# Kernel optimization log

Measured on AMD Instinct MI355X. Metric: run time of the kernel, lower is better.

## Reference

```python
import jax, jax.numpy as jnp
import numpy as np

N = 32768          # nodes
E = 131072         # edges
H = 4              # heads
RNA = 128          # rna_feature_dim
PROT = 32          # prot_feature_dim
F0 = 64            # num_features_per_layer[0] == [1]
CIN = F0 + PROT    # cross-path feature dim (96)
LRELU = 0.2


def _param(key, shape):
    return jax.random.normal(key, shape, dtype=jnp.float32) * 0.1


def setup_inputs() -> dict:
    key = jax.random.key(0)
    ks = jax.random.split(key, 20)
    return {
        "rna_data": jax.random.normal(ks[0], (N, RNA), dtype=jnp.float32),
        "prot_data": jax.random.normal(ks[1], (N, PROT), dtype=jnp.float32),
        "edge_index": jax.random.randint(ks[2], (2, E), 0, N, dtype=jnp.int32),
        "W_gat_proj": _param(ks[3], (RNA, F0)),
        "b_gat_proj": _param(ks[4], (F0,)),
        "W_gat_reproj": _param(ks[5], (F0, RNA)),
        "b_gat_reproj": _param(ks[6], (RNA,)),
        "Wg": _param(ks[7], (F0, H * F0)),
        "ag_src": _param(ks[8], (H, F0)),
        "ag_trg": _param(ks[9], (H, F0)),
        "bg": _param(ks[10], (F0,)),
        "W_cross_proj": _param(ks[11], (RNA + PROT, CIN)),
        "b_cross_proj": _param(ks[12], (CIN,)),
        "W_cross_reproj": _param(ks[13], (CIN, RNA + PROT)),
        "b_cross_reproj": _param(ks[14], (RNA + PROT,)),
        "Wc": _param(ks[15], (CIN, H * CIN)),
        "ac_src": _param(ks[16], (H, CIN)),
        "ac_trg": _param(ks[17], (H, CIN)),
        "bc": _param(ks[18], (CIN,)),
    }


def gat_layer(x, W, a_src, a_trg, bias, edge_index, softmax_on_src):
    """GATLayer with concat=False, activation=None, skip connection (in==out dim),
    dropout in eval mode. CrossAttnLayer groups the edge-softmax by src instead of trg."""
    n, f = x.shape
    src, trg = edge_index[0], edge_index[1]
    proj = (x @ W).reshape(n, H, f)                               # [N,H,F] lift targets
    s_src = jnp.einsum('nhf,hf->nh', proj, a_src)                 # [N,H]
    s_trg = jnp.einsum('nhf,hf->nh', proj, a_trg)                 # [N,H]
    scores = jax.nn.leaky_relu(s_src[src] + s_trg[trg], LRELU)    # [E,H] per-edge scores
    grp = src if softmax_on_src else trg
    ex = jnp.exp(scores - scores.max())                           # global-max shift (as in source)
    denom = jax.ops.segment_sum(ex, grp, num_segments=n)          # [N,H]
    attn = ex / (denom[grp] + 1e-16)                              # neighborhood-aware softmax [E,H]
    weighted = proj[src] * attn[:, :, None]                       # [E,H,F]
    out = jax.ops.segment_sum(weighted, trg, num_segments=n)      # scatter-add aggregate [N,H,F]
    out = out + x[:, None, :]                                     # direct skip (out_dim == in_dim)
    out = out.mean(axis=1) + bias                                 # concat=False -> head mean, + bias
    return out                                                    # activation=None (last layer)


def reference(rna_data, prot_data, edge_index,
              W_gat_proj, b_gat_proj, W_gat_reproj, b_gat_reproj,
              Wg, ag_src, ag_trg, bg,
              W_cross_proj, b_cross_proj, W_cross_reproj, b_cross_reproj,
              Wc, ac_src, ac_trg, bc):
    concat = jnp.concatenate([rna_data, prot_data], axis=1)       # [N, RNA+PROT]
    rna_p = rna_data @ W_gat_proj + b_gat_proj                    # [N, F0]
    cross_p = concat @ W_cross_proj + b_cross_proj                # [N, CIN]
    gat_out = gat_layer(rna_p, Wg, ag_src, ag_trg, bg, edge_index, False)    # [N, F0]
    cross_out = gat_layer(cross_p, Wc, ac_src, ac_trg, bc, edge_index, True)  # [N, CIN]
    # CrossAttnLayer's trailing view(-1, num_heads, num_out_features)
    cross_out = cross_out.reshape(-1, H, CIN)                     # [N/H, H, CIN]
    gat_final = gat_out @ W_gat_reproj + b_gat_reproj             # [N, RNA]
    cross_final = cross_out @ W_cross_reproj + b_cross_reproj     # [N/H, H, RNA+PROT]
    return gat_final, cross_final
```

## Files before the change

### kernel.cpp

```cpp
#include <hip/hip_runtime.h>
#include <hip/hip_bf16.h>

#define NN 32768
#define NE 131072
#define HH 4

constexpr float kLrelu = 0.2f;

using bf16x8 = __attribute__((ext_vector_type(8))) __bf16;
using f32x4  = __attribute__((ext_vector_type(4))) float;

__device__ inline short f2b(float f) {
    __hip_bfloat16 h = __float2bfloat16(f);
    return __builtin_bit_cast(short, h);
}
__device__ inline float b2f(short s) {
    __hip_bfloat16 h = __builtin_bit_cast(__hip_bfloat16, s);
    return __bfloat162float(h);
}
__device__ inline float blo(int u) {
    return __builtin_bit_cast(float, (int)(u << 16));
}
__device__ inline float bhi(int u) {
    return __builtin_bit_cast(float, (int)(u & 0xffff0000));
}
__device__ inline float lrexp(float x) {
    return __expf(x > 0.f ? x : kLrelu * x);
}

template<int K, int LDA, int OUTN, int BM, int BN, bool BF16OUT>
__device__ __forceinline__ void gemm_dev(
    const short* __restrict__ A, const short* __restrict__ Wt,
    const float* __restrict__ bias,
    float* __restrict__ Cf, short* __restrict__ Cb,
    short* lds, int bx, int by)
{
    constexpr int KP    = K + 8;
    constexpr int WM    = BM / 32;
    constexpr int WN    = 4 / WM;
    constexpr int WBN   = BN / WN;
    constexpr int CF    = WBN / 16;
    constexpr int CPR   = K / 8;
    constexpr int TOT   = (BM + BN) * KP;
    constexpr int SLICE = TOT / 4;

    short* As = lds;
    short* Bs = lds + BM * KP;

    const int tid  = threadIdx.x;
    const int wave = tid >> 6;
    const int lane = tid & 63;
    const int lr   = lane & 15;
    const int kb   = lane >> 4;
    const int wm   = wave % WM;
    const int wn   = wave / WM;
    const int row0 = bx * BM;
    const int col0 = by * BN;

    #pragma unroll
    for (int g = tid; g < BM * CPR; g += 256) {
        int r = g / CPR, c = g - r * CPR;
        bf16x8 v = *(const bf16x8*)(A + (size_t)(row0 + r) * LDA + c * 8);
        *(bf16x8*)(As + r * KP + c * 8) = v;
    }
    #pragma unroll
    for (int g = tid; g < BN * CPR; g += 256) {
        int r = g / CPR, c = g - r * CPR;
        bf16x8 v = *(const bf16x8*)(Wt + (size_t)(col0 + r) * K + c * 8);
        *(bf16x8*)(Bs + r * KP + c * 8) = v;
    }
    __syncthreads();

    f32x4 acc[2][CF] = {};
    #pragma unroll
    for (int k0 = 0; k0 < K; k0 += 32) {
        bf16x8 af0 = *(const bf16x8*)(As + (wm * 32 + lr     ) * KP + k0 + kb * 8);
        bf16x8 af1 = *(const bf16x8*)(As + (wm * 32 + lr + 16) * KP + k0 + kb * 8);
        #pragma unroll
        for (int cf = 0; cf < CF; ++cf) {
            bf16x8 bv = *(const bf16x8*)(Bs + (wn * WBN + cf * 16 + lr) * KP + k0 + kb * 8);
            acc[0][cf] = __builtin_amdgcn_mfma_f32_16x16x32_bf16(af0, bv, acc[0][cf], 0, 0, 0);
            acc[1][cf] = __builtin_amdgcn_mfma_f32_16x16x32_bf16(af1, bv, acc[1][cf], 0, 0, 0);
        }
    }

    #pragma unroll
    for (int mf = 0; mf < 2; ++mf) {
        __syncthreads();
        if constexpr (BF16OUT) {
            constexpr int LEP = WBN + 8;
            short* ep = lds + wave * SLICE;
            #pragma unroll
            for (int cf = 0; cf < CF; ++cf) {
                const int c  = cf * 16 + lr;
                const float bv = bias ? bias[col0 + wn * WBN + c] : 0.0f;
                #pragma unroll
                for (int j = 0; j < 4; ++j)
                    ep[(kb * 4 + j) * LEP + c] = f2b(acc[mf][cf][j] + bv);
            }
            __syncthreads();
            constexpr int CROW = WBN / 8;
            for (int g = lane; g < 16 * CROW; g += 64) {
                int r = g / CROW, cc = g - r * CROW;
                bf16x8 v = *(const bf16x8*)(ep + r * LEP + cc * 8);
                *(bf16x8*)(Cb + (size_t)(row0 + wm * 32 + mf * 16 + r) * OUTN
                              + col0 + wn * WBN + cc * 8) = v;
            }
        } else {
            constexpr int LEPF = WBN + 4;
            float* epf = (float*)(lds + wave * SLICE);
            #pragma unroll
            for (int cf = 0; cf < CF; ++cf) {
                const int c  = cf * 16 + lr;
                const float bv = bias ? bias[col0 + wn * WBN + c] : 0.0f;
                #pragma unroll
                for (int j = 0; j < 4; ++j)
                    epf[(kb * 4 + j) * LEPF + c] = acc[mf][cf][j] + bv;
            }
            __syncthreads();
            constexpr int CROWF = WBN / 4;
            for (int g = lane; g < 16 * CROWF; g += 64) {
                int r = g / CROWF, cc = g - r * CROWF;
                float4 v = *(const float4*)(epf + r * LEPF + cc * 4);
                *(float4*)(Cf + (size_t)(row0 + wm * 32 + mf * 16 + r) * OUTN
                              + col0 + wn * WBN + cc * 4) = v;
            }
        }
    }
}

template<int K1, int LDA1, int OUTN1, int BM1, int BN1, bool BO1,
         int K2, int LDA2, int OUTN2, int BM2, int BN2, bool BO2>
__global__ __launch_bounds__(256) void dual_gemm(
    const short* A1, const short* Wt1, const float* b1, float* Cf1, short* Cb1,
    int nbx1, int nby1,
    const short* A2, const short* Wt2, const float* b2, float* Cf2, short* Cb2,
    int nbx2, int nby2)
{
    constexpr int TOT1 = (BM1 + BN1) * (K1 + 8);
    constexpr int TOT2 = (BM2 + BN2) * (K2 + 8);
    constexpr int TOT  = TOT1 > TOT2 ? TOT1 : TOT2;
    __shared__ short lds[TOT];
    if (blockIdx.z == 0) {
        if ((int)blockIdx.x < nbx1 && (int)blockIdx.y < nby1)
            gemm_dev<K1, LDA1, OUTN1, BM1, BN1, BO1>(A1, Wt1, b1, Cf1, Cb1, lds,
                                                     blockIdx.x, blockIdx.y);
    } else {
        if ((int)blockIdx.x < nbx2 && (int)blockIdx.y < nby2)
            gemm_dev<K2, LDA2, OUTN2, BM2, BN2, BO2>(A2, Wt2, b2, Cf2, Cb2, lds,
                                                     blockIdx.x, blockIdx.y);
    }
}

template<int F>
__device__ inline void score_one(
    const short* __restrict__ proj_b,
    const float* __restrict__ a_src, const float* __restrict__ a_trg,
    float* __restrict__ ssrc, float* __restrict__ strg, int t)
{
    int n = t >> 2, h = t & 3;
    const int4* p = (const int4*)(proj_b + (size_t)n * (4 * F) + h * F);
    const float* as = a_src + h * F;
    const float* at = a_trg + h * F;
    float ss = 0.f, st = 0.f;
    #pragma unroll
    for (int c = 0; c < F / 8; ++c) {
        int4 v = p[c];
        int u[4] = { v.x, v.y, v.z, v.w };
        #pragma unroll
        for (int q = 0; q < 4; ++q) {
            float x0 = blo(u[q]), x1 = bhi(u[q]);
            ss += x0 * as[c * 8 + 2 * q] + x1 * as[c * 8 + 2 * q + 1];
            st += x0 * at[c * 8 + 2 * q] + x1 * at[c * 8 + 2 * q + 1];
        }
    }
    ssrc[t] = ss;
    strg[t] = st;
}

__global__ __launch_bounds__(256) void scores_both(
    const short* __restrict__ projG,
    const float* __restrict__ agsG, const float* __restrict__ agtG,
    float* __restrict__ ssrcG, float* __restrict__ strgG,
    const short* __restrict__ projC,
    const float* __restrict__ acsC, const float* __restrict__ actC,
    float* __restrict__ ssrcC, float* __restrict__ strgC)
{
    int t = blockIdx.x * 256 + threadIdx.x;
    if (t < NN * HH) score_one<64>(projG, agsG, agtG, ssrcG, strgG, t);
    else             score_one<96>(projC, acsC, actC, ssrcC, strgC, t - NN * HH);
}

__global__ __launch_bounds__(256) void prep_kernel(
    const float* __restrict__ rna, const float* __restrict__ prot,
    short* __restrict__ cb,
    const float* W0, const float* W1, const float* W2,
    const float* W3, const float* W4, const float* W5,
    short* T0, short* T1, short* T2, short* T3, short* T4, short* T5,
    int4* __restrict__ zero_p)
{
    const int bid = blockIdx.x;
    if (bid < 5120) {
        int t = bid * 256 + threadIdx.x;
        int n = t / 40, j = (t - n * 40) * 4;
        float4 v = (j < 128) ? *(const float4*)(rna  + (size_t)n * 128 + j)
                             : *(const float4*)(prot + (size_t)n * 32 + (j - 128));
        short4 o = { f2b(v.x), f2b(v.y), f2b(v.z), f2b(v.w) };
        *(short4*)(cb + (size_t)n * 160 + j) = o;
    } else if (bid < 5984) {
        int idx = bid - 5120;
        int wsel = idx / 144, sub = idx - wsel * 144;
        int K, N; const float* W; short* T;
        switch (wsel) {
            case 0: K = 128; N =  64; W = W0; T = T0; break;
            case 1: K =  64; N = 256; W = W1; T = T1; break;
            case 2: K =  64; N = 128; W = W2; T = T2; break;
            case 3: K = 160; N =  96; W = W3; T = T3; break;
            case 4: K =  96; N = 384; W = W4; T = T4; break;
            default:K =  96; N = 160; W = W5; T = T5; break;
        }
        int t = sub * 256 + threadIdx.x;
        if (t >= K * N) return;
        int n = t / K, k = t - n * K;
        T[t] = f2b(W[(size_t)k * N + n]);
    } else {
        zero_p[(bid - 5984) * 256 + threadIdx.x] = make_int4(0, 0, 0, 0);
    }
}

__global__ __launch_bounds__(256) void hist_dual(const int* __restrict__ ei,
                                                 int* __restrict__ deg_t,
                                                 int* __restrict__ deg_s)
{
    int e = blockIdx.x * 256 + threadIdx.x;
    if (e >= NE) return;
    atomicAdd(&deg_s[ei[e]], 1);
    atomicAdd(&deg_t[ei[NE + e]], 1);
}

__global__ __launch_bounds__(1024) void scan_dual(
    const int* __restrict__ deg_t, int* __restrict__ rowptr_t, int* __restrict__ cursor_t,
    const int* __restrict__ deg_s, int* __restrict__ rowptr_s, int* __restrict__ cursor_s)
{
    const int* deg    = blockIdx.x ? deg_s    : deg_t;
    int*       rowptr = blockIdx.x ? rowptr_s : rowptr_t;
    int*       cursor = blockIdx.x ? cursor_s : cursor_t;
    __shared__ int sums[1024];
    const int t = threadIdx.x;
    const int base = t * 32;
    int local[32];
    int s = 0;
    #pragma unroll
    for (int i = 0; i < 32; ++i) { local[i] = s; s += deg[base + i]; }
    sums[t] = s;
    __syncthreads();
    for (int off = 1; off < 1024; off <<= 1) {
        int v = (t >= off) ? sums[t - off] : 0;
        __syncthreads();
        sums[t] += v;
        __syncthreads();
    }
    const int prev = (t == 0) ? 0 : sums[t - 1];
    #pragma unroll
    for (int i = 0; i < 32; ++i) {
        rowptr[base + i] = prev + local[i];
        cursor[base + i] = prev + local[i];
    }
    if (t == 1023) rowptr[NN] = prev + s;
}

__global__ __launch_bounds__(256) void scatter_dual(
    const int* __restrict__ ei,
    int* __restrict__ cursor_t, int* __restrict__ csr_srcT,
    int* __restrict__ cursor_s, int* __restrict__ csr_trgS)
{
    int e = blockIdx.x * 256 + threadIdx.x;
    if (e >= NE) return;
    int s = ei[e], t = ei[NE + e];
    int st = atomicAdd(&cursor_t[t], 1);
    csr_srcT[st] = s;
    int ss = atomicAdd(&cursor_s[s], 1);
    csr_trgS[ss] = t;
}

__global__ __launch_bounds__(256) void den_src_kernel(
    const int* __restrict__ rowptr_s, const int* __restrict__ csr_trgS,
    const float* __restrict__ ssrc, const float* __restrict__ strg,
    float* __restrict__ recip)
{
    int n = blockIdx.x * 256 + threadIdx.x;
    if (n >= NN) return;
    const int beg = rowptr_s[n], end = rowptr_s[n + 1];
    const float4 sv = *(const float4*)(ssrc + 4 * (size_t)n);
    float d0 = 0.f, d1 = 0.f, d2 = 0.f, d3 = 0.f;
    for (int sl = beg; sl < end; ++sl) {
        const int t = csr_trgS[sl];
        const float4 tv = *(const float4*)(strg + 4 * (size_t)t);
        d0 += lrexp(sv.x + tv.x); d1 += lrexp(sv.y + tv.y);
        d2 += lrexp(sv.z + tv.z); d3 += lrexp(sv.w + tv.w);
    }
    *(float4*)(recip + 4 * (size_t)n) =
        make_float4(1.f / (d0 + 1e-16f), 1.f / (d1 + 1e-16f),
                    1.f / (d2 + 1e-16f), 1.f / (d3 + 1e-16f));
}

template<int F, bool GROUP_SRC>
__device__ __forceinline__ void agg_body(
    int f2, int node,
    const int* __restrict__ rowptr_t, const int* __restrict__ csr_srcT,
    const float* __restrict__ ssrc, const float* __restrict__ strg,
    const float* __restrict__ recip,
    const short* __restrict__ proj_b,
    const short* __restrict__ x_pb, const float* __restrict__ bias,
    short* __restrict__ aggb)
{
    const int beg = rowptr_t[node], end = rowptr_t[node + 1];
    const float4 stv = *(const float4*)(strg + 4 * (size_t)node);

    float a0 = 0.f, a1 = 0.f;
    float h0l = 0.f, h1l = 0.f, h2l = 0.f, h3l = 0.f;
    float h0h = 0.f, h1h = 0.f, h2h = 0.f, h3h = 0.f;
    float d0 = 0.f, d1 = 0.f, d2 = 0.f, d3 = 0.f;

    #pragma unroll 2
    for (int sl = beg; sl < end; ++sl) {
        const int s = csr_srcT[sl];
        const float4 sv = *(const float4*)(ssrc + 4 * (size_t)s);
        float e0 = lrexp(sv.x + stv.x);
        float e1 = lrexp(sv.y + stv.y);
        float e2 = lrexp(sv.z + stv.z);
        float e3 = lrexp(sv.w + stv.w);
        const short* p = proj_b + (size_t)s * (4 * F) + f2;
        const int u0 = *(const int*)(p);
        const int u1 = *(const int*)(p + F);
        const int u2 = *(const int*)(p + 2 * F);
        const int u3 = *(const int*)(p + 3 * F);
        if constexpr (GROUP_SRC) {
            const float4 rc = *(const float4*)(recip + 4 * (size_t)s);
            e0 *= rc.x; e1 *= rc.y; e2 *= rc.z; e3 *= rc.w;
            a0 += e0 * blo(u0) + e1 * blo(u1) + e2 * blo(u2) + e3 * blo(u3);
            a1 += e0 * bhi(u0) + e1 * bhi(u1) + e2 * bhi(u2) + e3 * bhi(u3);
        } else {
            d0 += e0; d1 += e1; d2 += e2; d3 += e3;
            h0l += e0 * blo(u0); h0h += e0 * bhi(u0);
            h1l += e1 * blo(u1); h1h += e1 * bhi(u1);
            h2l += e2 * blo(u2); h2h += e2 * bhi(u2);
            h3l += e3 * blo(u3); h3h += e3 * bhi(u3);
        }
    }
    if constexpr (!GROUP_SRC) {
        const float r0 = 1.f / (d0 + 1e-16f), r1 = 1.f / (d1 + 1e-16f);
        const float r2 = 1.f / (d2 + 1e-16f), r3 = 1.f / (d3 + 1e-16f);
        a0 = h0l * r0 + h1l * r1 + h2l * r2 + h3l * r3;
        a1 = h0h * r0 + h1h * r1 + h2h * r2 + h3h * r3;
    }
    const int o = node * F + f2;
    const int ux = *(const int*)(x_pb + o);
    const float v0 = a0 * 0.25f + blo(ux) + bias[f2];
    const float v1 = a1 * 0.25f + bhi(ux) + bias[f2 + 1];
    *(int*)(aggb + o) = (f2b(v0) & 0xffff) | ((int)f2b(v1) << 16);
}

#define GAT_BLKS 2731
__global__ __launch_bounds__(384) void aggregate_mega(
    const int* __restrict__ rowptr_t, const int* __restrict__ csr_srcT,
    const float* __restrict__ ssrcG, const float* __restrict__ strgG,
    const float* __restrict__ ssrcC, const float* __restrict__ strgC,
    const float* __restrict__ recip,
    const short* __restrict__ projG, const short* __restrict__ projC,
    const short* __restrict__ xG, const short* __restrict__ xC,
    const float* __restrict__ biasG, const float* __restrict__ biasC,
    short* __restrict__ aggG, short* __restrict__ aggC)
{
    const int bid = blockIdx.x;
    const int tid = threadIdx.x;
    if (bid < GAT_BLKS) {
        const int node = bid * 12 + tid / 32;
        const int f2   = (tid & 31) * 2;
        if (node >= NN) return;
        agg_body<64, false>(f2, node, rowptr_t, csr_srcT, ssrcG, strgG,
                            nullptr, projG, xG, biasG, aggG);
    } else {
        const int b    = bid - GAT_BLKS;
        const int node = b * 8 + tid / 48;
        const int f2   = (tid % 48) * 2;
        agg_body<96, true>(f2, node, rowptr_t, csr_srcT, ssrcC, strgC,
                           recip, projC, xC, biasC, aggC);
    }
}

extern "C" void kernel_launch(void* const* d_in, const int* in_sizes, int n_in,
                              void* d_out, int out_size, void* d_ws, size_t ws_size,
                              hipStream_t stream)
{
    const float* rna   = (const float*)d_in[0];
    const float* prot  = (const float*)d_in[1];
    const int*   ei    = (const int*)  d_in[2];
    const float* Wgp   = (const float*)d_in[3];
    const float* bgp   = (const float*)d_in[4];
    const float* Wgr   = (const float*)d_in[5];
    const float* bgr   = (const float*)d_in[6];
    const float* Wg    = (const float*)d_in[7];
    const float* ags   = (const float*)d_in[8];
    const float* agt   = (const float*)d_in[9];
    const float* bg    = (const float*)d_in[10];
    const float* Wcp   = (const float*)d_in[11];
    const float* bcp   = (const float*)d_in[12];
    const float* Wcr   = (const float*)d_in[13];
    const float* bcr   = (const float*)d_in[14];
    const float* Wc    = (const float*)d_in[15];
    const float* acs   = (const float*)d_in[16];
    const float* act   = (const float*)d_in[17];
    const float* bc    = (const float*)d_in[18];

    float* out_gat   = (float*)d_out;
    float* out_cross = out_gat + (size_t)NN * 128;

    float* ssrcG  = (float*)d_ws;
    float* strgG  = ssrcG + (size_t)NN * 4;
    float* ssrcC  = strgG + (size_t)NN * 4;
    float* strgC  = ssrcC + (size_t)NN * 4;
    float* recip  = strgC + (size_t)NN * 4;
    short* projG  = (short*)(recip + (size_t)NN * 4);
    short* projC  = projG + (size_t)NN * 256;
    short* cb     = projC + (size_t)NN * 384;
    short* x_pG   = cb    + (size_t)NN * 160;
    short* x_pC   = x_pG  + (size_t)NN * 64;
    short* aggG   = x_pC  + (size_t)NN * 96;
    short* aggC   = aggG  + (size_t)NN * 64;
    short* wt_gp  = aggC  + (size_t)NN * 96;
    short* wt_g   = wt_gp + 128 * 64;
    short* wt_gr  = wt_g  + 64 * 256;
    short* wt_cp  = wt_gr + 64 * 128;
    short* wt_c   = wt_cp + 160 * 96;
    short* wt_cr  = wt_c  + 96 * 384;
    int*   deg_t  = (int*)(wt_cr + 96 * 160);
    int*   deg_s  = deg_t  + NN;
    int*   cursor_t = deg_s  + NN;
    int*   cursor_s = cursor_t + NN;
    int*   rowptr_t = cursor_s + NN;
    int*   rowptr_s = rowptr_t + NN + 1;
    int*   csr_srcT = rowptr_s + NN + 1;
    int*   csr_trgS = csr_srcT + NE;

    prep_kernel<<<6048, 256, 0, stream>>>(rna, prot, cb,
                                          Wgp, Wg, Wgr, Wcp, Wc, Wcr,
                                          wt_gp, wt_g, wt_gr, wt_cp, wt_c, wt_cr,
                                          (int4*)deg_t);
    hist_dual<<<NE / 256, 256, 0, stream>>>(ei, deg_t, deg_s);
    scan_dual<<<2, 1024, 0, stream>>>(deg_t, rowptr_t, cursor_t, deg_s, rowptr_s, cursor_s);
    scatter_dual<<<NE / 256, 256, 0, stream>>>(ei, cursor_t, csr_srcT, cursor_s, csr_trgS);

    dual_gemm<128, 160,  64, 32,  64, true,
              160, 160,  96, 64,  96, true><<<dim3(1024, 1, 2), 256, 0, stream>>>(
        cb, wt_gp, bgp, nullptr, x_pG, 1024, 1,
        cb, wt_cp, bcp, nullptr, x_pC,  512, 1);

    dual_gemm< 64,  64, 256, 64, 128, true,
               96,  96, 384, 64, 128, true><<<dim3(512, 3, 2), 256, 0, stream>>>(
        x_pG, wt_g, nullptr, nullptr, projG, 512, 2,
        x_pC, wt_c, nullptr, nullptr, projC, 512, 3);

    scores_both<<<(2 * NN * HH) / 256, 256, 0, stream>>>(
        projG, ags, agt, ssrcG, strgG, projC, acs, act, ssrcC, strgC);
    den_src_kernel<<<NN / 256, 256, 0, stream>>>(rowptr_s, csr_trgS, ssrcC, strgC, recip);

    aggregate_mega<<<GAT_BLKS + NN / 8, 384, 0, stream>>>(
        rowptr_t, csr_srcT, ssrcG, strgG, ssrcC, strgC, recip,
        projG, projC, x_pG, x_pC, bg, bc, aggG, aggC);

    dual_gemm< 64,  64, 128, 64,  64, false,
               96,  96, 160, 64, 160, false><<<dim3(512, 2, 2), 256, 0, stream>>>(
        aggG, wt_gr, bgr, out_gat,   nullptr, 512, 2,
        aggC, wt_cr, bcr, out_cross, nullptr, 512, 1);
}
```

Before: 167.2 us.

## Split each node's edge loop across two thread halves in aggregation

The aggregation kernel now assigns two groups of lanes per node, each handling alternate incoming edges, then combines partial sums (via cross-lane shuffle for the GAT path and shared memory plus a block barrier for the cross path). This doubles the thread count and block count to expose more memory-level parallelism on the irregular gather. In exchange it adds reduction overhead, a __syncthreads, and half the lanes idle during the epilogue.

```diff
diff --git a/kernel.cpp b/kernel.cpp
--- a/kernel.cpp
+++ b/kernel.cpp
@@ -304,64 +304,7 @@
                     1.f / (d2 + 1e-16f), 1.f / (d3 + 1e-16f));
 }
 
-template<int F, bool GROUP_SRC>
-__device__ __forceinline__ void agg_body(
-    int f2, int node,
-    const int* __restrict__ rowptr_t, const int* __restrict__ csr_srcT,
-    const float* __restrict__ ssrc, const float* __restrict__ strg,
-    const float* __restrict__ recip,
-    const short* __restrict__ proj_b,
-    const short* __restrict__ x_pb, const float* __restrict__ bias,
-    short* __restrict__ aggb)
-{
-    const int beg = rowptr_t[node], end = rowptr_t[node + 1];
-    const float4 stv = *(const float4*)(strg + 4 * (size_t)node);
-
-    float a0 = 0.f, a1 = 0.f;
-    float h0l = 0.f, h1l = 0.f, h2l = 0.f, h3l = 0.f;
-    float h0h = 0.f, h1h = 0.f, h2h = 0.f, h3h = 0.f;
-    float d0 = 0.f, d1 = 0.f, d2 = 0.f, d3 = 0.f;
-
-    #pragma unroll 2
-    for (int sl = beg; sl < end; ++sl) {
-        const int s = csr_srcT[sl];
-        const float4 sv = *(const float4*)(ssrc + 4 * (size_t)s);
-        float e0 = lrexp(sv.x + stv.x);
-        float e1 = lrexp(sv.y + stv.y);
-        float e2 = lrexp(sv.z + stv.z);
-        float e3 = lrexp(sv.w + stv.w);
-        const short* p = proj_b + (size_t)s * (4 * F) + f2;
-        const int u0 = *(const int*)(p);
-        const int u1 = *(const int*)(p + F);
-        const int u2 = *(const int*)(p + 2 * F);
-        const int u3 = *(const int*)(p + 3 * F);
-        if constexpr (GROUP_SRC) {
-            const float4 rc = *(const float4*)(recip + 4 * (size_t)s);
-            e0 *= rc.x; e1 *= rc.y; e2 *= rc.z; e3 *= rc.w;
-            a0 += e0 * blo(u0) + e1 * blo(u1) + e2 * blo(u2) + e3 * blo(u3);
-            a1 += e0 * bhi(u0) + e1 * bhi(u1) + e2 * bhi(u2) + e3 * bhi(u3);
-        } else {
-            d0 += e0; d1 += e1; d2 += e2; d3 += e3;
-            h0l += e0 * blo(u0); h0h += e0 * bhi(u0);
-            h1l += e1 * blo(u1); h1h += e1 * bhi(u1);
-            h2l += e2 * blo(u2); h2h += e2 * bhi(u2);
-            h3l += e3 * blo(u3); h3h += e3 * bhi(u3);
-        }
-    }
-    if constexpr (!GROUP_SRC) {
-        const float r0 = 1.f / (d0 + 1e-16f), r1 = 1.f / (d1 + 1e-16f);
-        const float r2 = 1.f / (d2 + 1e-16f), r3 = 1.f / (d3 + 1e-16f);
-        a0 = h0l * r0 + h1l * r1 + h2l * r2 + h3l * r3;
-        a1 = h0h * r0 + h1h * r1 + h2h * r2 + h3h * r3;
-    }
-    const int o = node * F + f2;
-    const int ux = *(const int*)(x_pb + o);
-    const float v0 = a0 * 0.25f + blo(ux) + bias[f2];
-    const float v1 = a1 * 0.25f + bhi(ux) + bias[f2 + 1];
-    *(int*)(aggb + o) = (f2b(v0) & 0xffff) | ((int)f2b(v1) << 16);
-}
-
-#define GAT_BLKS 2731
+#define GAT_BLKS 5462
 __global__ __launch_bounds__(384) void aggregate_mega(
     const int* __restrict__ rowptr_t, const int* __restrict__ csr_srcT,
     const float* __restrict__ ssrcG, const float* __restrict__ strgG,
@@ -372,20 +315,97 @@
     const float* __restrict__ biasG, const float* __restrict__ biasC,
     short* __restrict__ aggG, short* __restrict__ aggC)
 {
+    __shared__ float red[2][192];
     const int bid = blockIdx.x;
     const int tid = threadIdx.x;
+
     if (bid < GAT_BLKS) {
-        const int node = bid * 12 + tid / 32;
-        const int f2   = (tid & 31) * 2;
+        const int node = bid * 6 + (tid >> 6);
         if (node >= NN) return;
-        agg_body<64, false>(f2, node, rowptr_t, csr_srcT, ssrcG, strgG,
-                            nullptr, projG, xG, biasG, aggG);
+        const int lane = tid & 63;
+        const int half = lane >> 5;
+        const int f2   = (lane & 31) * 2;
+        const int beg  = rowptr_t[node], end = rowptr_t[node + 1];
+        const float4 stv = *(const float4*)(strgG + 4 * (size_t)node);
+
+        float h0l = 0.f, h1l = 0.f, h2l = 0.f, h3l = 0.f;
+        float h0h = 0.f, h1h = 0.f, h2h = 0.f, h3h = 0.f;
+        float d0 = 0.f, d1 = 0.f, d2 = 0.f, d3 = 0.f;
+
+        for (int sl = beg + half; sl < end; sl += 2) {
+            const int s = csr_srcT[sl];
+            const float4 sv = *(const float4*)(ssrcG + 4 * (size_t)s);
+            const float e0 = lrexp(sv.x + stv.x);
+            const float e1 = lrexp(sv.y + stv.y);
+            const float e2 = lrexp(sv.z + stv.z);
+            const float e3 = lrexp(sv.w + stv.w);
+            const short* p = projG + (size_t)s * 256 + f2;
+            const int u0 = *(const int*)(p);
+            const int u1 = *(const int*)(p + 64);
+            const int u2 = *(const int*)(p + 128);
+            const int u3 = *(const int*)(p + 192);
+            d0 += e0; d1 += e1; d2 += e2; d3 += e3;
+            h0l += e0 * blo(u0); h0h += e0 * bhi(u0);
+            h1l += e1 * blo(u1); h1h += e1 * bhi(u1);
+            h2l += e2 * blo(u2); h2h += e2 * bhi(u2);
+            h3l += e3 * blo(u3); h3h += e3 * bhi(u3);
+        }
+        d0 += __shfl_xor(d0, 32); d1 += __shfl_xor(d1, 32);
+        d2 += __shfl_xor(d2, 32); d3 += __shfl_xor(d3, 32);
+        h0l += __shfl_xor(h0l, 32); h0h += __shfl_xor(h0h, 32);
+        h1l += __shfl_xor(h1l, 32); h1h += __shfl_xor(h1h, 32);
+        h2l += __shfl_xor(h2l, 32); h2h += __shfl_xor(h2h, 32);
+        h3l += __shfl_xor(h3l, 32); h3h += __shfl_xor(h3h, 32);
+        if (half == 0) {
+            const float r0 = 1.f / (d0 + 1e-16f), r1 = 1.f / (d1 + 1e-16f);
+            const float r2 = 1.f / (d2 + 1e-16f), r3 = 1.f / (d3 + 1e-16f);
+            const float a0 = h0l * r0 + h1l * r1 + h2l * r2 + h3l * r3;
+            const float a1 = h0h * r0 + h1h * r1 + h2h * r2 + h3h * r3;
+            const int o = node * 64 + f2;
+            const int ux = *(const int*)(xG + o);
+            const float v0 = a0 * 0.25f + blo(ux) + biasG[f2];
+            const float v1 = a1 * 0.25f + bhi(ux) + biasG[f2 + 1];
+            *(int*)(aggG + o) = (f2b(v0) & 0xffff) | ((int)f2b(v1) << 16);
+        }
     } else {
         const int b    = bid - GAT_BLKS;
-        const int node = b * 8 + tid / 48;
-        const int f2   = (tid % 48) * 2;
-        agg_body<96, true>(f2, node, rowptr_t, csr_srcT, ssrcC, strgC,
-                           recip, projC, xC, biasC, aggC);
+        const int nl   = tid / 96;
+        const int r    = tid - nl * 96;
+        const int half = r / 48;
+        const int f2   = (r - half * 48) * 2;
+        const int node = b * 4 + nl;
+        const int beg  = rowptr_t[node], end = rowptr_t[node + 1];
+        const float4 stv = *(const float4*)(strgC + 4 * (size_t)node);
+
+        float a0 = 0.f, a1 = 0.f;
+        for (int sl = beg + half; sl < end; sl += 2) {
+            const int s = csr_srcT[sl];
+            const float4 sv = *(const float4*)(ssrcC + 4 * (size_t)s);
+            const float4 rc = *(const float4*)(recip + 4 * (size_t)s);
+            const float e0 = lrexp(sv.x + stv.x) * rc.x;
+            const float e1 = lrexp(sv.y + stv.y) * rc.y;
+            const float e2 = lrexp(sv.z + stv.z) * rc.z;
+            const float e3 = lrexp(sv.w + stv.w) * rc.w;
+            const short* p = projC + (size_t)s * 384 + f2;
+            const int u0 = *(const int*)(p);
+            const int u1 = *(const int*)(p + 96);
+            const int u2 = *(const int*)(p + 192);
+            const int u3 = *(const int*)(p + 288);
+            a0 += e0 * blo(u0) + e1 * blo(u1) + e2 * blo(u2) + e3 * blo(u3);
+            a1 += e0 * bhi(u0) + e1 * bhi(u1) + e2 * bhi(u2) + e3 * bhi(u3);
+        }
+        const int slot = nl * 48 + (f2 >> 1);
+        if (half == 1) { red[0][slot] = a0; red[1][slot] = a1; }
+        __syncthreads();
+        if (half == 0) {
+            a0 += red[0][slot];
+            a1 += red[1][slot];
+            const int o = node * 96 + f2;
+            const int ux = *(const int*)(xC + o);
+            const float v0 = a0 * 0.25f + blo(ux) + biasC[f2];
+            const float v1 = a1 * 0.25f + bhi(ux) + biasC[f2 + 1];
+            *(int*)(aggC + o) = (f2b(v0) & 0xffff) | ((int)f2b(v1) << 16);
+        }
     }
 }
 
@@ -465,7 +485,7 @@
         projG, ags, agt, ssrcG, strgG, projC, acs, act, ssrcC, strgC);
     den_src_kernel<<<NN / 256, 256, 0, stream>>>(rowptr_s, csr_trgS, ssrcC, strgC, recip);
 
-    aggregate_mega<<<GAT_BLKS + NN / 8, 384, 0, stream>>>(
+    aggregate_mega<<<GAT_BLKS + NN / 4, 384, 0, stream>>>(
         rowptr_t, csr_srcT, ssrcG, strgG, ssrcC, strgC, recip,
         projG, projC, x_pG, x_pC, bg, bc, aggG, aggC);
 
```

After: 179.0 us. 7.0% more time.

## Precompute normalized per-edge attention coefficients in separate kernel before aggregation

Applied to the files above, without the earlier changes.

Adds an attn_both kernel that computes normalized softmax attention weights per edge, stored in CSR order for both the GAT and cross paths. The aggregation kernel then reads one float4 per edge instead of recomputing exp/leaky-relu and the softmax normalization in every feature lane. The aim is to remove redundant transcendental work that was repeated 32–48 times per edge. In exchange it adds a kernel launch, a second pass over edges for the GAT denominator, and 4 MB of extra global writes and reads.

```diff
diff --git a/kernel.cpp b/kernel.cpp
--- a/kernel.cpp
+++ b/kernel.cpp
@@ -304,55 +304,71 @@
                     1.f / (d2 + 1e-16f), 1.f / (d3 + 1e-16f));
 }
 
-template<int F, bool GROUP_SRC>
-__device__ __forceinline__ void agg_body(
+__global__ __launch_bounds__(256) void attn_both(
+    const int* __restrict__ rowptr_t, const int* __restrict__ csr_srcT,
+    const float* __restrict__ ssrcG, const float* __restrict__ strgG,
+    const float* __restrict__ ssrcC, const float* __restrict__ strgC,
+    const float* __restrict__ recip,
+    float* __restrict__ attnG, float* __restrict__ attnC)
+{
+    const int idx = blockIdx.x * 256 + threadIdx.x;
+    if (idx < NN) {
+        const int n = idx;
+        const int beg = rowptr_t[n], end = rowptr_t[n + 1];
+        const float4 tv = *(const float4*)(strgG + 4 * (size_t)n);
+        float d0 = 0.f, d1 = 0.f, d2 = 0.f, d3 = 0.f;
+        for (int sl = beg; sl < end; ++sl) {
+            const int s = csr_srcT[sl];
+            const float4 sv = *(const float4*)(ssrcG + 4 * (size_t)s);
+            d0 += lrexp(sv.x + tv.x); d1 += lrexp(sv.y + tv.y);
+            d2 += lrexp(sv.z + tv.z); d3 += lrexp(sv.w + tv.w);
+        }
+        const float r0 = 1.f / (d0 + 1e-16f), r1 = 1.f / (d1 + 1e-16f);
+        const float r2 = 1.f / (d2 + 1e-16f), r3 = 1.f / (d3 + 1e-16f);
+        for (int sl = beg; sl < end; ++sl) {
+            const int s = csr_srcT[sl];
+            const float4 sv = *(const float4*)(ssrcG + 4 * (size_t)s);
+            *(float4*)(attnG + 4 * (size_t)sl) =
+                make_float4(lrexp(sv.x + tv.x) * r0, lrexp(sv.y + tv.y) * r1,
+                            lrexp(sv.z + tv.z) * r2, lrexp(sv.w + tv.w) * r3);
+        }
+    } else {
+        const int n = idx - NN;
+        const int beg = rowptr_t[n], end = rowptr_t[n + 1];
+        const float4 tv = *(const float4*)(strgC + 4 * (size_t)n);
+        for (int sl = beg; sl < end; ++sl) {
+            const int s = csr_srcT[sl];
+            const float4 sv = *(const float4*)(ssrcC + 4 * (size_t)s);
+            const float4 rc = *(const float4*)(recip + 4 * (size_t)s);
+            *(float4*)(attnC + 4 * (size_t)sl) =
+                make_float4(lrexp(sv.x + tv.x) * rc.x, lrexp(sv.y + tv.y) * rc.y,
+                            lrexp(sv.z + tv.z) * rc.z, lrexp(sv.w + tv.w) * rc.w);
+        }
+    }
+}
+
+template<int F>
+__device__ __forceinline__ void agg_body2(
     int f2, int node,
     const int* __restrict__ rowptr_t, const int* __restrict__ csr_srcT,
-    const float* __restrict__ ssrc, const float* __restrict__ strg,
-    const float* __restrict__ recip,
+    const float* __restrict__ attn,
     const short* __restrict__ proj_b,
     const short* __restrict__ x_pb, const float* __restrict__ bias,
     short* __restrict__ aggb)
 {
     const int beg = rowptr_t[node], end = rowptr_t[node + 1];
-    const float4 stv = *(const float4*)(strg + 4 * (size_t)node);
-
     float a0 = 0.f, a1 = 0.f;
-    float h0l = 0.f, h1l = 0.f, h2l = 0.f, h3l = 0.f;
-    float h0h = 0.f, h1h = 0.f, h2h = 0.f, h3h = 0.f;
-    float d0 = 0.f, d1 = 0.f, d2 = 0.f, d3 = 0.f;
-
     #pragma unroll 2
     for (int sl = beg; sl < end; ++sl) {
         const int s = csr_srcT[sl];
-        const float4 sv = *(const float4*)(ssrc + 4 * (size_t)s);
-        float e0 = lrexp(sv.x + stv.x);
-        float e1 = lrexp(sv.y + stv.y);
-        float e2 = lrexp(sv.z + stv.z);
-        float e3 = lrexp(sv.w + stv.w);
+        const float4 av = *(const float4*)(attn + 4 * (size_t)sl);
         const short* p = proj_b + (size_t)s * (4 * F) + f2;
         const int u0 = *(const int*)(p);
         const int u1 = *(const int*)(p + F);
         const int u2 = *(const int*)(p + 2 * F);
         const int u3 = *(const int*)(p + 3 * F);
-        if constexpr (GROUP_SRC) {
-            const float4 rc = *(const float4*)(recip + 4 * (size_t)s);
-            e0 *= rc.x; e1 *= rc.y; e2 *= rc.z; e3 *= rc.w;
-            a0 += e0 * blo(u0) + e1 * blo(u1) + e2 * blo(u2) + e3 * blo(u3);
-            a1 += e0 * bhi(u0) + e1 * bhi(u1) + e2 * bhi(u2) + e3 * bhi(u3);
-        } else {
-            d0 += e0; d1 += e1; d2 += e2; d3 += e3;
-            h0l += e0 * blo(u0); h0h += e0 * bhi(u0);
-            h1l += e1 * blo(u1); h1h += e1 * bhi(u1);
-            h2l += e2 * blo(u2); h2h += e2 * bhi(u2);
-            h3l += e3 * blo(u3); h3h += e3 * bhi(u3);
-        }
-    }
-    if constexpr (!GROUP_SRC) {
-        const float r0 = 1.f / (d0 + 1e-16f), r1 = 1.f / (d1 + 1e-16f);
-        const float r2 = 1.f / (d2 + 1e-16f), r3 = 1.f / (d3 + 1e-16f);
-        a0 = h0l * r0 + h1l * r1 + h2l * r2 + h3l * r3;
-        a1 = h0h * r0 + h1h * r1 + h2h * r2 + h3h * r3;
+        a0 += av.x * blo(u0) + av.y * blo(u1) + av.z * blo(u2) + av.w * blo(u3);
+        a1 += av.x * bhi(u0) + av.y * bhi(u1) + av.z * bhi(u2) + av.w * bhi(u3);
     }
     const int o = node * F + f2;
     const int ux = *(const int*)(x_pb + o);
@@ -364,9 +380,7 @@
 #define GAT_BLKS 2731
 __global__ __launch_bounds__(384) void aggregate_mega(
     const int* __restrict__ rowptr_t, const int* __restrict__ csr_srcT,
-    const float* __restrict__ ssrcG, const float* __restrict__ strgG,
-    const float* __restrict__ ssrcC, const float* __restrict__ strgC,
-    const float* __restrict__ recip,
+    const float* __restrict__ attnG, const float* __restrict__ attnC,
     const short* __restrict__ projG, const short* __restrict__ projC,
     const short* __restrict__ xG, const short* __restrict__ xC,
     const float* __restrict__ biasG, const float* __restrict__ biasC,
@@ -378,14 +392,12 @@
         const int node = bid * 12 + tid / 32;
         const int f2   = (tid & 31) * 2;
         if (node >= NN) return;
-        agg_body<64, false>(f2, node, rowptr_t, csr_srcT, ssrcG, strgG,
-                            nullptr, projG, xG, biasG, aggG);
+        agg_body2<64>(f2, node, rowptr_t, csr_srcT, attnG, projG, xG, biasG, aggG);
     } else {
         const int b    = bid - GAT_BLKS;
         const int node = b * 8 + tid / 48;
         const int f2   = (tid % 48) * 2;
-        agg_body<96, true>(f2, node, rowptr_t, csr_srcT, ssrcC, strgC,
-                           recip, projC, xC, biasC, aggC);
+        agg_body2<96>(f2, node, rowptr_t, csr_srcT, attnC, projC, xC, biasC, aggC);
     }
 }
 
@@ -421,7 +433,9 @@
     float* ssrcC  = strgG + (size_t)NN * 4;
     float* strgC  = ssrcC + (size_t)NN * 4;
     float* recip  = strgC + (size_t)NN * 4;
-    short* projG  = (short*)(recip + (size_t)NN * 4);
+    float* attnG  = recip + (size_t)NN * 4;
+    float* attnC  = attnG + (size_t)NE * 4;
+    short* projG  = (short*)(attnC + (size_t)NE * 4);
     short* projC  = projG + (size_t)NN * 256;
     short* cb     = projC + (size_t)NN * 384;
     short* x_pG   = cb    + (size_t)NN * 160;
@@ -464,9 +478,11 @@
     scores_both<<<(2 * NN * HH) / 256, 256, 0, stream>>>(
         projG, ags, agt, ssrcG, strgG, projC, acs, act, ssrcC, strgC);
     den_src_kernel<<<NN / 256, 256, 0, stream>>>(rowptr_s, csr_trgS, ssrcC, strgC, recip);
+    attn_both<<<(2 * NN) / 256, 256, 0, stream>>>(
+        rowptr_t, csr_srcT, ssrcG, strgG, ssrcC, strgC, recip, attnG, attnC);
 
     aggregate_mega<<<GAT_BLKS + NN / 8, 384, 0, stream>>>(
-        rowptr_t, csr_srcT, ssrcG, strgG, ssrcC, strgC, recip,
+        rowptr_t, csr_srcT, attnG, attnC,
         projG, projC, x_pG, x_pC, bg, bc, aggG, aggC);
 
     dual_gemm< 64,  64, 128, 64,  64, false,
```

New measurement: 171.4 us. +2.5%, slower.
